# Kernel optimization log

Hardware: AMD Instinct MI355X
Metric: run time of the kernel (lower is better)

The kernel has to match this reference:

```python
import jax, jax.numpy as jnp
import numpy as np

NUM_HEADS = 16
NUM_KV_HEADS = 8
HEAD_DIM = 128
GATE_LOW_RANK = 16
GATE_NORMALIZER = 16.0
NORM_EPS = 1e-5
CHUNK = 64


def gla_chunk(q, k, v, g, chunk=CHUNK):
    """Chunkwise-parallel gated linear attention.
    q,k,v,g: [B,H,L,D]. Recurrence: S_t = diag(exp(g_t)) S_{t-1} + k_t^T v_t; o_t = q_t S_t.
    """
    B, H, L, D = q.shape
    n = L // chunk

    def rs(x):  # -> [n, B, H, C, D]
        return x.reshape(B, H, n, chunk, D).transpose(2, 0, 1, 3, 4)

    qc, kc, vc, gc = rs(q), rs(k), rs(v), rs(g)
    causal = jnp.tril(jnp.ones((chunk, chunk), dtype=bool))

    def step(S, inp):
        qt, kt, vt, gt = inp                      # [B,H,C,D]
        b = jnp.cumsum(gt, axis=-2)               # inclusive cumulative log-gates
        q_ = qt * jnp.exp(b)
        k_ = kt * jnp.exp(-b)
        # intra-chunk causal attention (diag included)
        A = jnp.einsum('bhid,bhjd->bhij', q_, k_)
        A = jnp.where(causal, A, 0.0)
        o = jnp.einsum('bhij,bhje->bhie', A, vt)
        # inter-chunk contribution from carried state
        o = o + jnp.einsum('bhid,bhde->bhie', q_, S)
        # state update to end of chunk
        k_end = kt * jnp.exp(b[..., -1:, :] - b)
        S_new = S * jnp.exp(b[..., -1, :])[..., None] + jnp.einsum('bhcd,bhce->bhde', k_end, vt)
        return S_new, o

    S0 = jnp.zeros((B, H, D, D), q.dtype)
    _, o = jax.lax.scan(step, S0, (qc, kc, vc, gc))
    return o.transpose(1, 2, 0, 3, 4).reshape(B, H, L, D)


def setup_inputs() -> dict:
    key = jax.random.key(0)
    ks = jax.random.split(key, 10)
    B, L, HID = 2, 2048, 2048
    KV = NUM_KV_HEADS * HEAD_DIM  # 1024
    w = 0.02
    return {
        'hidden_states': jax.random.normal(ks[0], (B, L, HID), jnp.float32),
        'Wq': jax.random.normal(ks[1], (HID, HID), jnp.float32) * w,
        'bq': jnp.zeros((HID,), jnp.float32),
        'Wk': jax.random.normal(ks[2], (HID, KV), jnp.float32) * w,
        'bk': jnp.zeros((KV,), jnp.float32),
        'Wv': jax.random.normal(ks[3], (HID, KV), jnp.float32) * w,
        'bv': jnp.zeros((KV,), jnp.float32),
        'Wg1': jax.random.normal(ks[4], (HID, GATE_LOW_RANK), jnp.float32) * w,
        'Wg2': jax.random.normal(ks[5], (GATE_LOW_RANK, KV), jnp.float32) * w,
        'bg2': jnp.zeros((KV,), jnp.float32),
        'g_norm_w': jnp.ones((HEAD_DIM,), jnp.float32),
        'Wo': jax.random.normal(ks[6], (HID, HID), jnp.float32) * w,
    }


def reference(hidden_states, Wq, bq, Wk, bk, Wv, bv, Wg1, Wg2, bg2, g_norm_w, Wo):
    B, L, HID = hidden_states.shape
    H, HKV, D = NUM_HEADS, NUM_KV_HEADS, HEAD_DIM
    n_rep = H // HKV

    q = jax.nn.relu(hidden_states @ Wq + bq)          # feature_map = relu
    k = jax.nn.relu(hidden_states @ Wk + bk)
    v = hidden_states @ Wv + bv
    gk = jax.nn.log_sigmoid((hidden_states @ Wg1) @ Wg2 + bg2) / GATE_NORMALIZER

    q = q.reshape(B, L, H, D).transpose(0, 2, 1, 3)    # [B,H,L,D]
    def to_heads(x):
        return x.reshape(B, L, HKV, D).transpose(0, 2, 1, 3)
    k, v, gk = to_heads(k), to_heads(v), to_heads(gk)  # [B,HKV,L,D]
    # GQA: repeat kv heads
    k = jnp.repeat(k, n_rep, axis=1)
    v = jnp.repeat(v, n_rep, axis=1)
    gk = jnp.repeat(gk, n_rep, axis=1)

    q = q * (D ** -0.5)                                # scale as in chunk_gla
    o = gla_chunk(q, k, v, gk)                         # [B,H,L,D]

    # per-head RMSNorm over head_dim
    o = o * jax.lax.rsqrt(jnp.mean(o * o, axis=-1, keepdims=True) + NORM_EPS) * g_norm_w
    o = o.transpose(0, 2, 1, 3).reshape(B, L, H * D)
    return o @ Wo
```

## Files before the change

### kernel.cpp

```cpp
#include <hip/hip_runtime.h>

typedef unsigned short u16;
typedef u16 u16x8 __attribute__((ext_vector_type(8)));
typedef u16 u16x4 __attribute__((ext_vector_type(4)));
typedef __bf16 bf16x8 __attribute__((ext_vector_type(8)));
typedef float f32x4 __attribute__((ext_vector_type(4)));

#define DEVI static __device__ __forceinline__

DEVI float b2f(u16 u){ union { unsigned u; float f; } c; c.u = ((unsigned)u) << 16; return c.f; }
DEVI u16 f2b(float f){ union { float f; unsigned u; } c; c.f = f;
  unsigned r = c.u + 0x7fffu + ((c.u >> 16) & 1u); return (u16)(r >> 16); }
DEVI void gload16(const void* g, void* l){
  __builtin_amdgcn_global_load_lds((const __attribute__((address_space(1))) void*)g,
                                   (__attribute__((address_space(3))) void*)l, 16, 0, 0);
}
DEVI f32x4 MFMA(bf16x8 a, bf16x8 b, f32x4 c){
  return __builtin_amdgcn_mfma_f32_16x16x32_bf16(a, b, c, 0, 0, 0);
}

constexpr size_t OFF_HB  = 0;
constexpr size_t OFF_WCT = OFF_HB  + (size_t)4096*2048*2;
constexpr size_t OFF_WOT = OFF_WCT + (size_t)4224*2048*2;
constexpr size_t OFF_QKV = OFF_WOT + (size_t)2048*2048*2;
constexpr size_t OFF_G1  = OFF_QKV + (size_t)4096*4096*2;
constexpr size_t OFF_G   = OFF_G1  + (size_t)4096*16*4;
constexpr size_t OFF_EB  = OFF_G   + (size_t)4096*1024*4;
constexpr size_t OFF_KD  = OFF_EB  + (size_t)4096*1024*2;
constexpr size_t OFF_T   = OFF_KD  + (size_t)4096*1024*2;
constexpr size_t OFF_DV  = OFF_T   + (size_t)2*8*32*128*128*2;
constexpr size_t OFF_SP  = OFF_DV  + (size_t)2*8*32*128*4;
constexpr size_t OFF_ON  = OFF_SP  + (size_t)2*8*32*128*128*2;

__global__ __launch_bounds__(256) void k_conv_h(const float* __restrict__ h,
                                                u16* __restrict__ hb, u16* __restrict__ padz){
  int idx = blockIdx.x*256 + threadIdx.x, stride = gridDim.x*256;
  for (int i = idx; i < 4096*2048/4; i += stride){
    float4 v = ((const float4*)h)[i];
    u16x4 o; o[0]=f2b(v.x); o[1]=f2b(v.y); o[2]=f2b(v.z); o[3]=f2b(v.w);
    ((u16x4*)hb)[i] = o;
  }
  for (int i = idx; i < 112*2048/4; i += stride){ u16x4 z = {0,0,0,0}; ((u16x4*)padz)[i] = z; }
}

__global__ __launch_bounds__(256) void k_transpose(const float* __restrict__ src, u16* __restrict__ dst,
                                                   int K, int N, int rowOff, int pitch){
  __shared__ float tile[64][65];
  int kb = blockIdx.y*64, nb = blockIdx.x*64;
  int t = threadIdx.x, x = t & 63, y0 = t >> 6;
#pragma unroll
  for (int i = 0; i < 16; i++){
    int y = y0 + i*4, k = kb + y, n = nb + x;
    tile[y][x] = (n < N) ? src[(size_t)k*N + n] : 0.f;
  }
  __syncthreads();
#pragma unroll
  for (int i = 0; i < 16; i++){
    int y = y0 + i*4, n = nb + y, k = kb + x;
    if (n < N) dst[(size_t)(rowOff + n)*pitch + k] = f2b(tile[x][y]);
  }
}

template<int MODE>
__global__ __launch_bounds__(256) void k_gemm(const u16* __restrict__ A, const u16* __restrict__ Bt,
                                              u16* __restrict__ Cq, float* __restrict__ Cg1,
                                              float* __restrict__ Cf,
                                              const float* __restrict__ bq, const float* __restrict__ bk,
                                              const float* __restrict__ bv){
  constexpr int Kd = 2048;
  __shared__ u16 lA[128*32];
  __shared__ u16 lB[128*32];
  int nt = blockIdx.x, mt = blockIdx.y;
  int t = threadIdx.x, w = t >> 6, l = t & 63;
  size_t aBase = (size_t)(mt*128 + (t>>2))*Kd + (t&3)*8;
  size_t bBase = (size_t)(nt*128 + (t>>2))*Kd + (t&3)*8;
  int wm = (w>>1)*64, wn = (w&1)*64;
  f32x4 acc[4][4] = {};
  u16* lA0 = &lA[w*512]; u16* lA1 = &lA[2048 + w*512];
  u16* lB0 = &lB[w*512]; u16* lB1 = &lB[2048 + w*512];
  for (int k0 = 0; k0 < Kd; k0 += 32){
    gload16(A + aBase + k0, lA0);
    gload16(A + aBase + (size_t)64*Kd + k0, lA1);
    gload16(Bt + bBase + k0, lB0);
    gload16(Bt + bBase + (size_t)64*Kd + k0, lB1);
    __syncthreads();
    bf16x8 af[4], bfv[4];
#pragma unroll
    for (int mi = 0; mi < 4; mi++) af[mi]  = *(const bf16x8*)&lA[(wm + mi*16 + (l&15))*32 + (l>>4)*8];
#pragma unroll
    for (int ni = 0; ni < 4; ni++) bfv[ni] = *(const bf16x8*)&lB[(wn + ni*16 + (l&15))*32 + (l>>4)*8];
#pragma unroll
    for (int mi = 0; mi < 4; mi++)
#pragma unroll
      for (int ni = 0; ni < 4; ni++)
        acc[mi][ni] = MFMA(af[mi], bfv[ni], acc[mi][ni]);
    __syncthreads();
  }
  int iLoc = (l>>4)*4, jc = l & 15;
  if (MODE == 0){
#pragma unroll
    for (int ni = 0; ni < 4; ni++){
      int n0 = nt*128 + wn + ni*16;
      int n = n0 + jc;
      int kind; float bias = 0.f;
      if (n0 < 2048){ kind = 0; bias = bq[n]; }
      else if (n0 < 3072){ kind = 1; bias = bk[n - 2048]; }
      else if (n0 < 4096){ kind = 2; bias = bv[n - 3072]; }
      else if (n0 == 4096){ kind = 3; }
      else { kind = 4; }
      if (kind == 4) continue;
#pragma unroll
      for (int mi = 0; mi < 4; mi++){
        int m = mt*128 + wm + mi*16 + iLoc;
#pragma unroll
        for (int rr = 0; rr < 4; rr++){
          float x = acc[mi][ni][rr];
          int row = m + rr;
          if (kind == 0)      Cq[(size_t)row*4096 + n] = f2b(fmaxf(x + bias, 0.f) * 0.08838834764831845f);
          else if (kind == 1) Cq[(size_t)row*4096 + n] = f2b(fmaxf(x + bias, 0.f));
          else if (kind == 2) Cq[(size_t)row*4096 + n] = f2b(x + bias);
          else                Cg1[(size_t)row*16 + (n - 4096)] = x;
        }
      }
    }
  } else {
#pragma unroll
    for (int ni = 0; ni < 4; ni++){
      int n = nt*128 + wn + ni*16 + jc;
#pragma unroll
      for (int mi = 0; mi < 4; mi++){
        int m = mt*128 + wm + mi*16 + iLoc;
#pragma unroll
        for (int rr = 0; rr < 4; rr++) Cf[(size_t)(m+rr)*2048 + n] = acc[mi][ni][rr];
      }
    }
  }
}

__global__ __launch_bounds__(256) void k_gates(const float* __restrict__ G1, const float* __restrict__ Wg2,
                                               const float* __restrict__ bg2, float* __restrict__ g){
  __shared__ float w2[16*1024];
  __shared__ float bb[1024];
  __shared__ float g1l[256];
  int t = threadIdx.x;
  for (int i = t; i < 4096; i += 256) ((float4*)w2)[i] = ((const float4*)Wg2)[i];
  ((float4*)bb)[t] = ((const float4*)bg2)[t];
  int tok0 = blockIdx.x*16;
  g1l[t] = G1[(size_t)tok0*16 + t];
  __syncthreads();
  int c0 = t*4;
  for (int tk = 0; tk < 16; tk++){
    float4 a = *(const float4*)&bb[c0];
#pragma unroll
    for (int r = 0; r < 16; r++){
      float gv = g1l[tk*16 + r];
      float4 wr = *(const float4*)&w2[r*1024 + c0];
      a.x += gv*wr.x; a.y += gv*wr.y; a.z += gv*wr.z; a.w += gv*wr.w;
    }
    float4 o;
    o.x = (fminf(a.x,0.f) - log1pf(expf(-fabsf(a.x)))) * 0.0625f;
    o.y = (fminf(a.y,0.f) - log1pf(expf(-fabsf(a.y)))) * 0.0625f;
    o.z = (fminf(a.z,0.f) - log1pf(expf(-fabsf(a.z)))) * 0.0625f;
    o.w = (fminf(a.w,0.f) - log1pf(expf(-fabsf(a.w)))) * 0.0625f;
    *(float4*)&g[(size_t)(tok0+tk)*1024 + c0] = o;
  }
}

__global__ __launch_bounds__(256) void k_phaseA(const float* __restrict__ g, const u16* __restrict__ QKV,
                                                u16* __restrict__ eb, u16* __restrict__ kd,
                                                u16* __restrict__ T, float* __restrict__ Dv){
  __shared__ float gb[64*128];
  __shared__ u16 keT[128*72];
  __shared__ u16 vT [128*72];
  int c = blockIdx.x, kvh = blockIdx.y, b = blockIdx.z;
  int t = threadIdx.x;
  int tok0 = b*2048 + c*64;
#pragma unroll
  for (int r = 0; r < 8; r++){
    int idx4 = r*256 + t;
    int i = idx4 >> 5, c4 = idx4 & 31;
    ((float4*)gb)[i*32 + c4] = *(const float4*)&g[(size_t)(tok0+i)*1024 + kvh*128 + c4*4];
  }
  __syncthreads();
  if (t < 128){
    float run = 0.f;
    for (int i = 0; i < 64; i++){ run += gb[i*128 + t]; gb[i*128 + t] = run; }
    Dv[((size_t)(b*8+kvh)*32 + c)*128 + t] = expf(run);
  }
  __syncthreads();
  int d0 = (t&15)*8;
  float blast[8];
#pragma unroll
  for (int j = 0; j < 8; j++) blast[j] = gb[63*128 + d0 + j];
#pragma unroll
  for (int r = 0; r < 4; r++){
    int i = (t>>4) + r*16;
    u16x8 kv_ = *(const u16x8*)&QKV[(size_t)(tok0+i)*4096 + 2048 + kvh*128 + d0];
    u16x8 vv  = *(const u16x8*)&QKV[(size_t)(tok0+i)*4096 + 3072 + kvh*128 + d0];
    u16x8 ebv, kdv;
#pragma unroll
    for (int j = 0; j < 8; j++){
      float bcur = gb[i*128 + d0 + j];
      float kf = b2f(kv_[j]);
      ebv[j] = f2b(expf(bcur));
      kdv[j] = f2b(kf * expf(-bcur));
      keT[(d0+j)*72 + i] = f2b(kf * expf(blast[j] - bcur));
      vT [(d0+j)*72 + i] = vv[j];
    }
    *(u16x8*)&eb[(size_t)(tok0+i)*1024 + kvh*128 + d0] = ebv;
    *(u16x8*)&kd[(size_t)(tok0+i)*1024 + kvh*128 + d0] = kdv;
  }
  __syncthreads();
  int w = t>>6, l = t&63;
  f32x4 acc[2][8] = {};
#pragma unroll
  for (int ks = 0; ks < 2; ks++){
    bf16x8 af[2];
#pragma unroll
    for (int ti = 0; ti < 2; ti++)
      af[ti] = *(const bf16x8*)&keT[(w*32 + ti*16 + (l&15))*72 + ks*32 + (l>>4)*8];
#pragma unroll
    for (int tj = 0; tj < 8; tj++){
      bf16x8 bf_ = *(const bf16x8*)&vT[(tj*16 + (l&15))*72 + ks*32 + (l>>4)*8];
#pragma unroll
      for (int ti = 0; ti < 2; ti++) acc[ti][tj] = MFMA(af[ti], bf_, acc[ti][tj]);
    }
  }
  size_t tbase = ((size_t)(b*8+kvh)*32 + c)*16384;
#pragma unroll
  for (int ti = 0; ti < 2; ti++)
#pragma unroll
    for (int tj = 0; tj < 8; tj++)
#pragma unroll
      for (int rr = 0; rr < 4; rr++){
        int d = w*32 + ti*16 + (l>>4)*4 + rr, e = tj*16 + (l&15);
        T[tbase + d*128 + e] = f2b(acc[ti][tj][rr]);
      }
}

__global__ __launch_bounds__(256) void k_phaseB(const u16* __restrict__ T, const float* __restrict__ Dv,
                                                u16* __restrict__ SP){
  __shared__ u16 sl[16*128];
  int es = blockIdx.x, kvh = blockIdx.y, b = blockIdx.z;
  int t = threadIdx.x;
  size_t bh = (size_t)(b*8 + kvh);
  float S[8] = {0,0,0,0,0,0,0,0};
  for (int c = 0; c < 32; c++){
#pragma unroll
    for (int r = 0; r < 8; r++){
      int idx = r*256 + t, d = idx>>4, el = idx&15;
      sl[el*128 + d] = f2b(S[r]);
    }
    __syncthreads();
    size_t spb = (bh*32 + c)*16384 + (size_t)es*2048;
    *(u16x8*)&SP[spb + t*8] = *(const u16x8*)&sl[t*8];
    size_t tb  = (bh*32 + c)*16384;
    size_t dvb = (bh*32 + c)*128;
#pragma unroll
    for (int r = 0; r < 8; r++){
      int idx = r*256 + t, d = idx>>4, el = idx&15;
      float tv = b2f(T[tb + d*128 + es*16 + el]);
      S[r] = S[r]*Dv[dvb + d] + tv;
    }
    __syncthreads();
  }
}

__global__ __launch_bounds__(256) void k_phaseC(const u16* __restrict__ QKV, const u16* __restrict__ eb,
                                                const u16* __restrict__ kd, const u16* __restrict__ SP,
                                                const float* __restrict__ gnw, u16* __restrict__ onrm){
  __shared__ u16 kl[64*128];
  __shared__ u16 sl[64*72];
  __shared__ u16 vT[128*72];
  int c = blockIdx.x, h = blockIdx.y, b = blockIdx.z;
  int kvh = h >> 1;
  int t = threadIdx.x, w = t>>6, l = t&63;
  int tok0 = b*2048 + c*64;
#pragma unroll
  for (int is = 0; is < 4; is++){
    int row = (t>>4) + is*16;
    int d0s = 8*((t&15) ^ (row&7));
    gload16(&kd[(size_t)(tok0+row)*1024 + kvh*128 + d0s], &kl[is*2048 + w*512]);
  }
  int d0v = (t&15)*8;
#pragma unroll
  for (int r = 0; r < 4; r++){
    int i = (t>>4) + r*16;
    u16x8 vv = *(const u16x8*)&QKV[(size_t)(tok0+i)*4096 + 3072 + kvh*128 + d0v];
#pragma unroll
    for (int jj = 0; jj < 8; jj++) vT[(d0v+jj)*72 + i] = vv[jj];
  }
  bf16x8 aq[4];
  {
    int i = w*16 + (l&15);
#pragma unroll
    for (int kt = 0; kt < 4; kt++){
      int dq = kt*32 + (l>>4)*8;
      u16x8 qv = *(const u16x8*)&QKV[(size_t)(tok0+i)*4096 + h*128 + dq];
      u16x8 ev = *(const u16x8*)&eb[(size_t)(tok0+i)*1024 + kvh*128 + dq];
      u16x8 o;
#pragma unroll
      for (int jj = 0; jj < 8; jj++) o[jj] = f2b(b2f(qv[jj]) * b2f(ev[jj]));
      aq[kt] = __builtin_bit_cast(bf16x8, o);
    }
  }
  __syncthreads();
  f32x4 accs[4] = {};
#pragma unroll
  for (int kt = 0; kt < 4; kt++){
#pragma unroll
    for (int jt = 0; jt < 4; jt++){
      int j = jt*16 + (l&15);
      int byte_ = j*256 + ((2*(kt*32 + (l>>4)*8)) ^ ((j&7)<<4));
      bf16x8 bk_ = *(const bf16x8*)((const char*)kl + byte_);
      accs[jt] = MFMA(aq[kt], bk_, accs[jt]);
    }
  }
#pragma unroll
  for (int jt = 0; jt < 4; jt++)
#pragma unroll
    for (int rr = 0; rr < 4; rr++){
      int i = w*16 + (l>>4)*4 + rr;
      int j = jt*16 + (l&15);
      sl[i*72 + j] = f2b((i >= j) ? accs[jt][rr] : 0.f);
    }
  f32x4 acco[8] = {};
  size_t spb = ((size_t)(b*8+kvh)*32 + c)*16384;
#pragma unroll
  for (int kt = 0; kt < 4; kt++){
#pragma unroll
    for (int et = 0; et < 8; et++){
      int e = et*16 + (l&15);
      int dd = kt*32 + (l>>4)*8;
      bf16x8 bs = *(const bf16x8*)&SP[spb + (size_t)e*128 + dd];
      acco[et] = MFMA(aq[kt], bs, acco[et]);
    }
  }
#pragma unroll
  for (int kt2 = 0; kt2 < 2; kt2++){
    int i = w*16 + (l&15);
    bf16x8 as = *(const bf16x8*)&sl[i*72 + kt2*32 + (l>>4)*8];
#pragma unroll
    for (int et = 0; et < 8; et++){
      bf16x8 bv_ = *(const bf16x8*)&vT[(et*16 + (l&15))*72 + kt2*32 + (l>>4)*8];
      acco[et] = MFMA(as, bv_, acco[et]);
    }
  }
  float gw[8];
#pragma unroll
  for (int et = 0; et < 8; et++) gw[et] = gnw[et*16 + (l&15)];
#pragma unroll
  for (int rr = 0; rr < 4; rr++){
    int i = w*16 + (l>>4)*4 + rr;
    float ss = 0.f;
#pragma unroll
    for (int et = 0; et < 8; et++){ float x = acco[et][rr]; ss += x*x; }
    ss += __shfl_xor(ss, 1); ss += __shfl_xor(ss, 2);
    ss += __shfl_xor(ss, 4); ss += __shfl_xor(ss, 8);
    float sc = rsqrtf(ss*(1.f/128.f) + 1e-5f);
#pragma unroll
    for (int et = 0; et < 8; et++){
      int e = et*16 + (l&15);
      onrm[(size_t)(tok0+i)*2048 + h*128 + e] = f2b(acco[et][rr]*sc*gw[et]);
    }
  }
}

extern "C" void kernel_launch(void* const* d_in, const int* in_sizes, int n_in,
                              void* d_out, int out_size, void* d_ws, size_t ws_size,
                              hipStream_t stream){
  (void)in_sizes; (void)n_in; (void)out_size; (void)ws_size;
  const float* h   = (const float*)d_in[0];
  const float* Wq  = (const float*)d_in[1];
  const float* bq  = (const float*)d_in[2];
  const float* Wk  = (const float*)d_in[3];
  const float* bk  = (const float*)d_in[4];
  const float* Wv  = (const float*)d_in[5];
  const float* bv  = (const float*)d_in[6];
  const float* Wg1 = (const float*)d_in[7];
  const float* Wg2 = (const float*)d_in[8];
  const float* bg2 = (const float*)d_in[9];
  const float* gnw = (const float*)d_in[10];
  const float* Wo  = (const float*)d_in[11];
  float* out = (float*)d_out;
  char* ws = (char*)d_ws;
  u16*   hb   = (u16*)  (ws + OFF_HB);
  u16*   wct  = (u16*)  (ws + OFF_WCT);
  u16*   wot  = (u16*)  (ws + OFF_WOT);
  u16*   qkv  = (u16*)  (ws + OFF_QKV);
  float* g1   = (float*)(ws + OFF_G1);
  float* gbuf = (float*)(ws + OFF_G);
  u16*   ebuf = (u16*)  (ws + OFF_EB);
  u16*   kdb  = (u16*)  (ws + OFF_KD);
  u16*   Tb   = (u16*)  (ws + OFF_T);
  float* Dvb  = (float*)(ws + OFF_DV);
  u16*   SPb  = (u16*)  (ws + OFF_SP);
  u16*   onb  = (u16*)  (ws + OFF_ON);

  k_conv_h<<<2048, 256, 0, stream>>>(h, hb, wct + (size_t)4112*2048);
  k_transpose<<<dim3(32,32), 256, 0, stream>>>(Wq,  wct, 2048, 2048,    0, 2048);
  k_transpose<<<dim3(16,32), 256, 0, stream>>>(Wk,  wct, 2048, 1024, 2048, 2048);
  k_transpose<<<dim3(16,32), 256, 0, stream>>>(Wv,  wct, 2048, 1024, 3072, 2048);
  k_transpose<<<dim3( 1,32), 256, 0, stream>>>(Wg1, wct, 2048,   16, 4096, 2048);
  k_transpose<<<dim3(32,32), 256, 0, stream>>>(Wo,  wot, 2048, 2048,    0, 2048);
  k_gemm<0><<<dim3(33,32), 256, 0, stream>>>(hb, wct, qkv, g1, nullptr, bq, bk, bv);
  k_gates<<<256, 256, 0, stream>>>(g1, Wg2, bg2, gbuf);
  k_phaseA<<<dim3(32,8,2), 256, 0, stream>>>(gbuf, qkv, ebuf, kdb, Tb, Dvb);
  k_phaseB<<<dim3(8,8,2), 256, 0, stream>>>(Tb, Dvb, SPb);
  k_phaseC<<<dim3(32,16,2), 256, 0, stream>>>(qkv, ebuf, kdb, SPb, gnw, onb);
  k_gemm<1><<<dim3(16,32), 256, 0, stream>>>(onb, wot, nullptr, nullptr, out, nullptr, nullptr, nullptr);
}
```

Baseline: 478.8 us.

## Replace GEMMs with 256-wide tiled, 4-stage pipelined, swizzled LDS kernels

Replaces the 128x128 single-buffered GEMM with a 512-thread kernel using 256x256 (QKV) and 128x256 (output) tiles. It keeps a 4-deep ring of global-to-LDS async loads with explicit vmcnt waits, XOR-swizzles the LDS layout to avoid bank conflicts, remaps block IDs for locality, and raises priority around the MFMA loop. The low-rank gate projection moves out of the fused GEMM into a separate small dot-product kernel, which removes the padded extra N tile and the Wg1 transpose. This costs more LDS and registers per block, and the launch grid is sized exactly to one wave of blocks.

Result: slower. 503.1 us (+5.1%).

```diff
diff --git a/kernel.cpp b/kernel.cpp
--- a/kernel.cpp
+++ b/kernel.cpp
@@ -18,6 +18,8 @@
 DEVI f32x4 MFMA(bf16x8 a, bf16x8 b, f32x4 c){
   return __builtin_amdgcn_mfma_f32_16x16x32_bf16(a, b, c, 0, 0, 0);
 }
+#define WAITV(n) asm volatile("s_waitcnt vmcnt(" #n ")" ::: "memory")
+#define WAITL0()  asm volatile("s_waitcnt lgkmcnt(0)" ::: "memory")
 
 constexpr size_t OFF_HB  = 0;
 constexpr size_t OFF_WCT = OFF_HB  + (size_t)4096*2048*2;
@@ -32,15 +34,13 @@
 constexpr size_t OFF_SP  = OFF_DV  + (size_t)2*8*32*128*4;
 constexpr size_t OFF_ON  = OFF_SP  + (size_t)2*8*32*128*128*2;
 
-__global__ __launch_bounds__(256) void k_conv_h(const float* __restrict__ h,
-                                                u16* __restrict__ hb, u16* __restrict__ padz){
+__global__ __launch_bounds__(256) void k_conv_h(const float* __restrict__ h, u16* __restrict__ hb){
   int idx = blockIdx.x*256 + threadIdx.x, stride = gridDim.x*256;
   for (int i = idx; i < 4096*2048/4; i += stride){
     float4 v = ((const float4*)h)[i];
     u16x4 o; o[0]=f2b(v.x); o[1]=f2b(v.y); o[2]=f2b(v.z); o[3]=f2b(v.w);
     ((u16x4*)hb)[i] = o;
   }
-  for (int i = idx; i < 112*2048/4; i += stride){ u16x4 z = {0,0,0,0}; ((u16x4*)padz)[i] = z; }
 }
 
 __global__ __launch_bounds__(256) void k_transpose(const float* __restrict__ src, u16* __restrict__ dst,
@@ -61,80 +61,133 @@
   }
 }
 
-template<int MODE>
-__global__ __launch_bounds__(256) void k_gemm(const u16* __restrict__ A, const u16* __restrict__ Bt,
-                                              u16* __restrict__ Cq, float* __restrict__ Cg1,
-                                              float* __restrict__ Cf,
-                                              const float* __restrict__ bq, const float* __restrict__ bk,
-                                              const float* __restrict__ bv){
-  constexpr int Kd = 2048;
-  __shared__ u16 lA[128*32];
-  __shared__ u16 lB[128*32];
-  int nt = blockIdx.x, mt = blockIdx.y;
+template<int BM, int MODE>
+__global__ __launch_bounds__(512, 2) void gemm256(const u16* __restrict__ A, const u16* __restrict__ Bt,
+                                                  u16* __restrict__ Cq, float* __restrict__ Cf,
+                                                  const float* __restrict__ bq, const float* __restrict__ bk,
+                                                  const float* __restrict__ bv){
+  constexpr int NT = 64;
+  constexpr int MI = BM/32;
+  constexpr int ALOADS = BM/128;
+  constexpr int NTN = (MODE==0) ? 16 : 8;
+  __shared__ u16 sA[4*BM*32];
+  __shared__ u16 sB[4*256*32];
+  int id = blockIdx.x;
+  int swz = (id & 7)*32 + (id >> 3);
+  int mt = swz / NTN, nt = swz % NTN;
   int t = threadIdx.x, w = t >> 6, l = t & 63;
-  size_t aBase = (size_t)(mt*128 + (t>>2))*Kd + (t&3)*8;
-  size_t bBase = (size_t)(nt*128 + (t>>2))*Kd + (t&3)*8;
-  int wm = (w>>1)*64, wn = (w&1)*64;
-  f32x4 acc[4][4] = {};
-  u16* lA0 = &lA[w*512]; u16* lA1 = &lA[2048 + w*512];
-  u16* lB0 = &lB[w*512]; u16* lB1 = &lB[2048 + w*512];
-  for (int k0 = 0; k0 < Kd; k0 += 32){
-    gload16(A + aBase + k0, lA0);
-    gload16(A + aBase + (size_t)64*Kd + k0, lA1);
-    gload16(Bt + bBase + k0, lB0);
-    gload16(Bt + bBase + (size_t)64*Kd + k0, lB1);
-    __syncthreads();
-    bf16x8 af[4], bfv[4];
-#pragma unroll
-    for (int mi = 0; mi < 4; mi++) af[mi]  = *(const bf16x8*)&lA[(wm + mi*16 + (l&15))*32 + (l>>4)*8];
-#pragma unroll
-    for (int ni = 0; ni < 4; ni++) bfv[ni] = *(const bf16x8*)&lB[(wn + ni*16 + (l&15))*32 + (l>>4)*8];
-#pragma unroll
-    for (int mi = 0; mi < 4; mi++)
+  int wr = w >> 2, wc = w & 3;
+  int mRow0 = mt*BM, nCol0 = nt*256;
+  const u16* srcA[ALOADS]; const u16* srcB[2];
+#pragma unroll
+  for (int i = 0; i < ALOADS; i++){
+    int S = t + i*512, r = S>>2, g = (S&3) ^ ((r>>2)&3);
+    srcA[i] = A + (size_t)(mRow0 + r)*2048 + g*8;
+  }
+#pragma unroll
+  for (int i = 0; i < 2; i++){
+    int S = t + i*512, r = S>>2, g = (S&3) ^ ((r>>2)&3);
+    srcB[i] = Bt + (size_t)(nCol0 + r)*2048 + g*8;
+  }
+  auto ISSUE = [&](int T){
+    int buf = T & 3;
+    u16* dA = sA + buf*(BM*32);
+    u16* dB = sB + buf*(256*32);
+#pragma unroll
+    for (int i = 0; i < ALOADS; i++) gload16(srcA[i] + T*32, dA + (i*512 + w*64)*8);
+#pragma unroll
+    for (int i = 0; i < 2; i++)      gload16(srcB[i] + T*32, dB + (i*512 + w*64)*8);
+  };
+  f32x4 acc[MI][4] = {};
+  ISSUE(0); ISSUE(1); ISSUE(2);
+  for (int T = 0; T < NT; ++T){
+    if (T + 3 < NT) ISSUE(T + 3);
+    if constexpr (BM == 256){
+      if (T < NT-3)       WAITV(12);
+      else if (T == NT-3) WAITV(8);
+      else if (T == NT-2) WAITV(4);
+      else                WAITV(0);
+    } else {
+      if (T < NT-3)       WAITV(9);
+      else if (T == NT-3) WAITV(6);
+      else if (T == NT-2) WAITV(3);
+      else                WAITV(0);
+    }
+    __builtin_amdgcn_s_barrier();
+    const u16* bufA = sA + (T&3)*(BM*32);
+    const u16* bufB = sB + (T&3)*(256*32);
+    bf16x8 bfr[4], afr[MI];
+#pragma unroll
+    for (int ni = 0; ni < 4; ni++){
+      int r = wc*64 + ni*16 + (l&15);
+      int p = (l>>4) ^ ((r>>2)&3);
+      bfr[ni] = *(const bf16x8*)&bufB[(r*4 + p)*8];
+    }
+#pragma unroll
+    for (int mi = 0; mi < MI; mi++){
+      int r = wr*(BM/2) + mi*16 + (l&15);
+      int p = (l>>4) ^ ((r>>2)&3);
+      afr[mi] = *(const bf16x8*)&bufA[(r*4 + p)*8];
+    }
+    __builtin_amdgcn_s_setprio(1);
+#pragma unroll
+    for (int mi = 0; mi < MI; mi++)
 #pragma unroll
       for (int ni = 0; ni < 4; ni++)
-        acc[mi][ni] = MFMA(af[mi], bfv[ni], acc[mi][ni]);
-    __syncthreads();
+        acc[mi][ni] = MFMA(afr[mi], bfr[ni], acc[mi][ni]);
+    __builtin_amdgcn_s_setprio(0);
+    WAITL0();
+    __builtin_amdgcn_s_barrier();
   }
   int iLoc = (l>>4)*4, jc = l & 15;
   if (MODE == 0){
 #pragma unroll
     for (int ni = 0; ni < 4; ni++){
-      int n0 = nt*128 + wn + ni*16;
+      int n0 = nCol0 + wc*64 + ni*16;
       int n = n0 + jc;
-      int kind; float bias = 0.f;
+      int kind; float bias;
       if (n0 < 2048){ kind = 0; bias = bq[n]; }
       else if (n0 < 3072){ kind = 1; bias = bk[n - 2048]; }
-      else if (n0 < 4096){ kind = 2; bias = bv[n - 3072]; }
-      else if (n0 == 4096){ kind = 3; }
-      else { kind = 4; }
-      if (kind == 4) continue;
-#pragma unroll
-      for (int mi = 0; mi < 4; mi++){
-        int m = mt*128 + wm + mi*16 + iLoc;
+      else { kind = 2; bias = bv[n - 3072]; }
+#pragma unroll
+      for (int mi = 0; mi < MI; mi++){
+        int m = mRow0 + wr*(BM/2) + mi*16 + iLoc;
 #pragma unroll
         for (int rr = 0; rr < 4; rr++){
-          float x = acc[mi][ni][rr];
+          float x = acc[mi][ni][rr] + bias;
           int row = m + rr;
-          if (kind == 0)      Cq[(size_t)row*4096 + n] = f2b(fmaxf(x + bias, 0.f) * 0.08838834764831845f);
-          else if (kind == 1) Cq[(size_t)row*4096 + n] = f2b(fmaxf(x + bias, 0.f));
-          else if (kind == 2) Cq[(size_t)row*4096 + n] = f2b(x + bias);
-          else                Cg1[(size_t)row*16 + (n - 4096)] = x;
+          if (kind == 0)      Cq[(size_t)row*4096 + n] = f2b(fmaxf(x, 0.f) * 0.08838834764831845f);
+          else if (kind == 1) Cq[(size_t)row*4096 + n] = f2b(fmaxf(x, 0.f));
+          else                Cq[(size_t)row*4096 + n] = f2b(x);
         }
       }
     }
   } else {
 #pragma unroll
     for (int ni = 0; ni < 4; ni++){
-      int n = nt*128 + wn + ni*16 + jc;
-#pragma unroll
-      for (int mi = 0; mi < 4; mi++){
-        int m = mt*128 + wm + mi*16 + iLoc;
+      int n = nCol0 + wc*64 + ni*16 + jc;
+#pragma unroll
+      for (int mi = 0; mi < MI; mi++){
+        int m = mRow0 + wr*(BM/2) + mi*16 + iLoc;
 #pragma unroll
         for (int rr = 0; rr < 4; rr++) Cf[(size_t)(m+rr)*2048 + n] = acc[mi][ni][rr];
       }
     }
   }
+}
+
+__global__ __launch_bounds__(256) void k_g1(const u16* __restrict__ hb, const float* __restrict__ Wg1,
+                                            float* __restrict__ G1){
+  int t = threadIdx.x;
+  int tok = blockIdx.x*16 + (t>>4), j = t & 15;
+  const u16* hr = hb + (size_t)tok*2048;
+  float s = 0.f;
+  for (int k = 0; k < 2048; k += 8){
+    u16x8 hv = *(const u16x8*)&hr[k];
+#pragma unroll
+    for (int u = 0; u < 8; u++) s += b2f(hv[u]) * Wg1[(k+u)*16 + j];
+  }
+  G1[(size_t)tok*16 + j] = s;
 }
 
 __global__ __launch_bounds__(256) void k_gates(const float* __restrict__ G1, const float* __restrict__ Wg2,
@@ -397,16 +450,16 @@
   u16*   SPb  = (u16*)  (ws + OFF_SP);
   u16*   onb  = (u16*)  (ws + OFF_ON);
 
-  k_conv_h<<<2048, 256, 0, stream>>>(h, hb, wct + (size_t)4112*2048);
+  k_conv_h<<<2048, 256, 0, stream>>>(h, hb);
   k_transpose<<<dim3(32,32), 256, 0, stream>>>(Wq,  wct, 2048, 2048,    0, 2048);
   k_transpose<<<dim3(16,32), 256, 0, stream>>>(Wk,  wct, 2048, 1024, 2048, 2048);
   k_transpose<<<dim3(16,32), 256, 0, stream>>>(Wv,  wct, 2048, 1024, 3072, 2048);
-  k_transpose<<<dim3( 1,32), 256, 0, stream>>>(Wg1, wct, 2048,   16, 4096, 2048);
   k_transpose<<<dim3(32,32), 256, 0, stream>>>(Wo,  wot, 2048, 2048,    0, 2048);
-  k_gemm<0><<<dim3(33,32), 256, 0, stream>>>(hb, wct, qkv, g1, nullptr, bq, bk, bv);
+  gemm256<256,0><<<256, 512, 0, stream>>>(hb, wct, qkv, nullptr, bq, bk, bv);
+  k_g1<<<256, 256, 0, stream>>>(hb, Wg1, g1);
   k_gates<<<256, 256, 0, stream>>>(g1, Wg2, bg2, gbuf);
   k_phaseA<<<dim3(32,8,2), 256, 0, stream>>>(gbuf, qkv, ebuf, kdb, Tb, Dvb);
   k_phaseB<<<dim3(8,8,2), 256, 0, stream>>>(Tb, Dvb, SPb);
   k_phaseC<<<dim3(32,16,2), 256, 0, stream>>>(qkv, ebuf, kdb, SPb, gnw, onb);
-  k_gemm<1><<<dim3(16,32), 256, 0, stream>>>(onb, wot, nullptr, nullptr, out, nullptr, nullptr, nullptr);
-}
+  gemm256<128,1><<<256, 512, 0, stream>>>(onb, wot, nullptr, out, nullptr, nullptr, nullptr);
+}
```
